# Performance work log

Measured on AMD Instinct MI355X. Metric: run time of the kernel, lower is better.

The kernel has to match this reference:

```python
import jax, jax.numpy as jnp
import numpy as np

V, E, H, O = 50257, 1024, 1024, 50257

def setup_inputs() -> dict:
    key = jax.random.key(0)
    ks = jax.random.split(key, 10)
    s = lambda k, shape, sc=0.02: jax.random.normal(k, shape, dtype=jnp.float32) * sc
    return {
        "inp": jax.random.randint(ks[0], (1,), 0, V),
        "h_0": s(ks[1], (1, H), 1.0),
        "c_0": s(ks[2], (1, H), 1.0),
        "emb": s(ks[3], (V, E)),
        "Wx": s(ks[4], (4 * H, E)),   # stacked [f,i,o,z] input->hidden weights
        "bx": jnp.zeros((4 * H,), jnp.float32),
        "Wh": s(ks[5], (4 * H, H)),   # stacked [f,i,o,z] hidden->hidden weights
        "bh": jnp.zeros((4 * H,), jnp.float32),
        "alpha": jnp.ones((4, H), jnp.float32),
        "beta1": jnp.ones((4, H), jnp.float32),
        "beta2": jnp.ones((4, H), jnp.float32),
        "Wdec": s(ks[6], (O, H)),
        "bdec": jnp.zeros((O,), jnp.float32),
    }

def reference(inp, h_0, c_0, emb, Wx, bx, Wh, bh, alpha, beta1, beta2, Wdec, bdec):
    x = emb[inp]                                   # [1, E] embedding lookup
    gx = (x @ Wx.T + bx).reshape(1, 4, H)          # stacked fx, ix, ox, zx
    gh = (h_0 @ Wh.T + bh).reshape(1, 4, H)        # stacked fh, ih, oh, zh
    m = alpha * gx * gh + beta1 * gx + beta2 * gh  # multiplicative integration, [1,4,H]
    f_g = jax.nn.sigmoid(m[:, 0])
    i_g = jax.nn.sigmoid(m[:, 1])
    o_g = jax.nn.sigmoid(m[:, 2])
    z_t = jnp.tanh(m[:, 3])
    cx = f_g * c_0 + i_g * z_t
    hx = o_g * jnp.tanh(cx)
    out = hx.reshape(1, -1) @ Wdec.T + bdec        # [1, O]
    return (out, hx, cx)
```

## Files before the change

kernel.cpp:

```cpp
#include <hip/hip_runtime.h>
#include <hip/hip_bf16.h>

#define VOCAB 50257
#define EMB   1024
#define HID   1024
#define OUTV  50257


__device__ __forceinline__ float wave_reduce(float v) {
    #pragma unroll
    for (int off = 32; off > 0; off >>= 1) v += __shfl_xor(v, off);
    return v;
}

__device__ __forceinline__ float dot4(float4 a, float4 b) {
    return a.x * b.x + a.y * b.y + a.z * b.z + a.w * b.w;
}

__global__ __launch_bounds__(256) void k_gates_cell(
        const int* __restrict__ inp,
        const float* __restrict__ emb,
        const float* __restrict__ Wx, const float* __restrict__ bx,
        const float* __restrict__ Wh, const float* __restrict__ bh,
        const float* __restrict__ h0,
        const float* __restrict__ alpha, const float* __restrict__ beta1,
        const float* __restrict__ beta2,
        const float* __restrict__ c0,
        float* __restrict__ hx_ws,
        float* __restrict__ out_hx, float* __restrict__ out_cx) {
    __shared__ float m_s[4];

    const int g    = threadIdx.x >> 6;
    const int lane = threadIdx.x & 63;
    const int j    = blockIdx.x;
    const int r    = g * HID + j;

    const size_t x_off = (size_t)inp[0] * (size_t)EMB;
    const float* wx_row = Wx + (size_t)r * EMB;
    const float* wh_row = Wh + (size_t)r * HID;

    float accx = 0.f, acch = 0.f;
    #pragma unroll
    for (int s = 0; s < 4; ++s) {
        const int c = s * 256 + lane * 4;
        float4 wxv = *(const float4*)(wx_row + c);
        float4 xv  = *(const float4*)(emb + x_off + c);
        float4 whv = *(const float4*)(wh_row + c);
        float4 hv  = *(const float4*)(h0 + c);
        accx += dot4(wxv, xv);
        acch += dot4(whv, hv);
    }
    accx = wave_reduce(accx);
    acch = wave_reduce(acch);

    if (lane == 0) {
        float gx = accx + bx[r];
        float gh = acch + bh[r];
        m_s[g] = alpha[r] * gx * gh + beta1[r] * gx + beta2[r] * gh;
    }
    __syncthreads();

    if (threadIdx.x == 0) {
        float fg = 1.f / (1.f + expf(-m_s[0]));
        float ig = 1.f / (1.f + expf(-m_s[1]));
        float og = 1.f / (1.f + expf(-m_s[2]));
        float zt = tanhf(m_s[3]);
        float c  = fg * c0[j] + ig * zt;
        float h  = og * tanhf(c);
        hx_ws[j]  = h;
        out_hx[j] = h;
        out_cx[j] = c;
    }
}

__global__ __launch_bounds__(256) void k_dec(
        const float* __restrict__ hx_ws,
        const float* __restrict__ Wdec, const float* __restrict__ bdec,
        float* __restrict__ out) {
    __shared__ float xs[HID];
    for (int t = threadIdx.x; t < HID; t += 256) xs[t] = hx_ws[t];
    __syncthreads();

    const int wave = threadIdx.x >> 6;
    const int lane = threadIdx.x & 63;
    const int r = blockIdx.x * 4 + wave;
    if (r >= OUTV) return;

    const float* wrow = Wdec + (size_t)r * HID;
    float acc = 0.f;
    #pragma unroll
    for (int s = 0; s < 4; ++s) {
        const int c = s * 256 + lane * 4;
        float4 w = *(const float4*)(wrow + c);
        float4 x = *(const float4*)(xs + c);
        acc += dot4(w, x);
    }
    acc = wave_reduce(acc);
    if (lane == 0) out[r] = acc + bdec[r];
}

extern "C" void kernel_launch(void* const* d_in, const int* in_sizes, int n_in,
                              void* d_out, int out_size, void* d_ws, size_t ws_size,
                              hipStream_t stream) {
    const int*   inp   = (const int*)d_in[0];
    const float* h0    = (const float*)d_in[1];
    const float* c0    = (const float*)d_in[2];
    const float* emb   = (const float*)d_in[3];
    const float* Wx    = (const float*)d_in[4];
    const float* bx    = (const float*)d_in[5];
    const float* Wh    = (const float*)d_in[6];
    const float* bh    = (const float*)d_in[7];
    const float* alpha = (const float*)d_in[8];
    const float* beta1 = (const float*)d_in[9];
    const float* beta2 = (const float*)d_in[10];
    const float* Wdec  = (const float*)d_in[11];
    const float* bdec  = (const float*)d_in[12];

    float* out   = (float*)d_out;
    float* hx_ws = (float*)d_ws;

    k_gates_cell<<<1024, 256, 0, stream>>>(inp, emb, Wx, bx, Wh, bh, h0,
                                           alpha, beta1, beta2, c0,
                                           hx_ws, out + OUTV, out + OUTV + HID);
    k_dec<<<(OUTV + 3) / 4, 256, 0, stream>>>(hx_ws, Wdec, bdec, out);
}
```

Before: 42.88 us.

## Fuse LSTM cell and decoder into one persistent kernel with grid barrier

Merges the gate/cell kernel and the decoder GEMV into a single launch of 1024 blocks that synchronize through a global atomic counter barrier. After the barrier, each wave walks decoder rows in a grid-stride loop. This removes the second kernel launch and its ramp-up gap, but adds a memset, a spin-wait on every block, and fewer waves streaming Wdec, which may lower memory-level parallelism. It also depends on all 1024 blocks being resident at once, which the launch bounds hint is meant to ensure.

```diff
diff --git a/kernel.cpp b/kernel.cpp
--- a/kernel.cpp
+++ b/kernel.cpp
@@ -17,7 +17,7 @@
     return a.x * b.x + a.y * b.y + a.z * b.z + a.w * b.w;
 }
 
-__global__ __launch_bounds__(256) void k_gates_cell(
+__global__ __launch_bounds__(256, 4) void k_milstm_fused(
         const int* __restrict__ inp,
         const float* __restrict__ emb,
         const float* __restrict__ Wx, const float* __restrict__ bx,
@@ -26,77 +26,86 @@
         const float* __restrict__ alpha, const float* __restrict__ beta1,
         const float* __restrict__ beta2,
         const float* __restrict__ c0,
+        const float* __restrict__ Wdec, const float* __restrict__ bdec,
+        float* __restrict__ out,
         float* __restrict__ hx_ws,
-        float* __restrict__ out_hx, float* __restrict__ out_cx) {
+        unsigned* __restrict__ bar) {
     __shared__ float m_s[4];
+    __shared__ float xs[HID];
 
     const int g    = threadIdx.x >> 6;
     const int lane = threadIdx.x & 63;
     const int j    = blockIdx.x;
     const int r    = g * HID + j;
 
-    const size_t x_off = (size_t)inp[0] * (size_t)EMB;
-    const float* wx_row = Wx + (size_t)r * EMB;
-    const float* wh_row = Wh + (size_t)r * HID;
+    {
+        const size_t x_off = (size_t)inp[0] * (size_t)EMB;
+        const float* wx_row = Wx + (size_t)r * EMB;
+        const float* wh_row = Wh + (size_t)r * HID;
 
-    float accx = 0.f, acch = 0.f;
-    #pragma unroll
-    for (int s = 0; s < 4; ++s) {
-        const int c = s * 256 + lane * 4;
-        float4 wxv = *(const float4*)(wx_row + c);
-        float4 xv  = *(const float4*)(emb + x_off + c);
-        float4 whv = *(const float4*)(wh_row + c);
-        float4 hv  = *(const float4*)(h0 + c);
-        accx += dot4(wxv, xv);
-        acch += dot4(whv, hv);
+        float accx = 0.f, acch = 0.f;
+        #pragma unroll
+        for (int s = 0; s < 4; ++s) {
+            const int c = s * 256 + lane * 4;
+            float4 wxv = *(const float4*)(wx_row + c);
+            float4 xv  = *(const float4*)(emb + x_off + c);
+            float4 whv = *(const float4*)(wh_row + c);
+            float4 hv  = *(const float4*)(h0 + c);
+            accx += dot4(wxv, xv);
+            acch += dot4(whv, hv);
+        }
+        accx = wave_reduce(accx);
+        acch = wave_reduce(acch);
+
+        if (lane == 0) {
+            float gx = accx + bx[r];
+            float gh = acch + bh[r];
+            m_s[g] = alpha[r] * gx * gh + beta1[r] * gx + beta2[r] * gh;
+        }
+        __syncthreads();
+
+        if (threadIdx.x == 0) {
+            float fg = 1.f / (1.f + expf(-m_s[0]));
+            float ig = 1.f / (1.f + expf(-m_s[1]));
+            float og = 1.f / (1.f + expf(-m_s[2]));
+            float zt = tanhf(m_s[3]);
+            float c  = fg * c0[j] + ig * zt;
+            float h  = og * tanhf(c);
+            hx_ws[j]            = h;
+            out[OUTV + j]       = h;
+            out[OUTV + HID + j] = c;
+        }
     }
-    accx = wave_reduce(accx);
-    acch = wave_reduce(acch);
 
-    if (lane == 0) {
-        float gx = accx + bx[r];
-        float gh = acch + bh[r];
-        m_s[g] = alpha[r] * gx * gh + beta1[r] * gx + beta2[r] * gh;
+    if (threadIdx.x == 0) {
+        __threadfence();
+        atomicAdd(bar, 1u);
+        unsigned spins = 0;
+        while (__hip_atomic_load(bar, __ATOMIC_RELAXED,
+                                 __HIP_MEMORY_SCOPE_AGENT) < 1024u) {
+            if (++spins > 100000000u) break;
+        }
+        __threadfence();
     }
     __syncthreads();
 
-    if (threadIdx.x == 0) {
-        float fg = 1.f / (1.f + expf(-m_s[0]));
-        float ig = 1.f / (1.f + expf(-m_s[1]));
-        float og = 1.f / (1.f + expf(-m_s[2]));
-        float zt = tanhf(m_s[3]);
-        float c  = fg * c0[j] + ig * zt;
-        float h  = og * tanhf(c);
-        hx_ws[j]  = h;
-        out_hx[j] = h;
-        out_cx[j] = c;
-    }
-}
-
-__global__ __launch_bounds__(256) void k_dec(
-        const float* __restrict__ hx_ws,
-        const float* __restrict__ Wdec, const float* __restrict__ bdec,
-        float* __restrict__ out) {
-    __shared__ float xs[HID];
     for (int t = threadIdx.x; t < HID; t += 256) xs[t] = hx_ws[t];
     __syncthreads();
 
-    const int wave = threadIdx.x >> 6;
-    const int lane = threadIdx.x & 63;
-    const int r = blockIdx.x * 4 + wave;
-    if (r >= OUTV) return;
-
-    const float* wrow = Wdec + (size_t)r * HID;
-    float acc = 0.f;
-    #pragma unroll
-    for (int s = 0; s < 4; ++s) {
-        const int c = s * 256 + lane * 4;
-        float4 w = *(const float4*)(wrow + c);
-        float4 x = *(const float4*)(xs + c);
-        acc += dot4(w, x);
+    const int wave_gid = blockIdx.x * 4 + g;
+    for (int row = wave_gid; row < OUTV; row += 4096) {
+        const float* wrow = Wdec + (size_t)row * HID;
+        float acc = 0.f;
+        #pragma unroll
+        for (int s = 0; s < 4; ++s) {
+            const int c = s * 256 + lane * 4;
+            float4 w = *(const float4*)(wrow + c);
+            float4 x = *(const float4*)(xs + c);
+            acc += dot4(w, x);
+        }
+        acc = wave_reduce(acc);
+        if (lane == 0) out[row] = acc + bdec[row];
     }
-    acc = wave_reduce(acc);
-    if (lane == 0) out[r] = acc + bdec[r];
 }
 
 extern "C" void kernel_launch(void* const* d_in, const int* in_sizes, int n_in,
@@ -117,10 +126,12 @@
     const float* bdec  = (const float*)d_in[12];
 
     float* out   = (float*)d_out;
-    float* hx_ws = (float*)d_ws;
+    float*    hx_ws = (float*)d_ws;
+    unsigned* bar   = (unsigned*)((char*)d_ws + 4096);
 
-    k_gates_cell<<<1024, 256, 0, stream>>>(inp, emb, Wx, bx, Wh, bh, h0,
-                                           alpha, beta1, beta2, c0,
-                                           hx_ws, out + OUTV, out + OUTV + HID);
-    k_dec<<<(OUTV + 3) / 4, 256, 0, stream>>>(hx_ws, Wdec, bdec, out);
+    hipMemsetAsync(bar, 0, sizeof(unsigned), stream);
+
+    k_milstm_fused<<<1024, 256, 0, stream>>>(inp, emb, Wx, bx, Wh, bh, h0,
+                                             alpha, beta1, beta2, c0,
+                                             Wdec, bdec, out, hx_ws, bar);
 }
```

New measurement: 127.6 us. +197.5%, slower.
